# Performance work log

Measured on AMD Instinct MI355X. Metric: run time of the kernel, lower is better.

The kernel has to match this reference:

```python
import jax, jax.numpy as jnp
import numpy as np

N_VIEW = 4
N_USER = 1_000_000
N_PRODUCT = 500_000
EMB = 64


def setup_inputs() -> dict:
    key = jax.random.key(0)
    k1, k2, k3, k4 = jax.random.split(key, 4)
    return {
        "view_users": jax.random.normal(k1, (N_VIEW, N_USER, EMB), dtype=jnp.float32),
        "view_products": jax.random.normal(k2, (N_VIEW, N_PRODUCT, EMB), dtype=jnp.float32),
        "user_view_weight": jax.random.normal(k3, (1, N_VIEW), dtype=jnp.float32),
        "product_view_weight": jax.random.normal(k4, (1, N_VIEW), dtype=jnp.float32),
    }


def reference(view_users, view_products, user_view_weight, product_view_weight):
    # softmax over the view axis (dim=1 of the [1, n_view] weight)
    uw = jax.nn.softmax(user_view_weight, axis=1)[0]      # [n_view]
    pw = jax.nn.softmax(product_view_weight, axis=1)[0]   # [n_view]
    # fused weighted sum over views: sum_v w[v] * items[v]
    users = jnp.einsum("v,vne->ne", uw, view_users)       # [n_user, emb]
    products = jnp.einsum("v,vme->me", pw, view_products) # [n_product, emb]
    return (users, products)
```

## Files before the change

### kernel.cpp

```cpp
#include <hip/hip_runtime.h>


typedef float f4 __attribute__((ext_vector_type(4)));

constexpr long long N_USER = 1000000LL;
constexpr long long N_PRODUCT = 500000LL;
constexpr int EMB = 64;

constexpr int BLOCK = 256;
constexpr int GRID = 2048;
constexpr int STRIDE = BLOCK * GRID;
constexpr int NU4 = (int)(N_USER * EMB / 4);
constexpr int NP4 = (int)(N_PRODUCT * EMB / 4);
constexpr int U_ITERS = NU4 / STRIDE;
constexpr int U_REM = NU4 % STRIDE;
constexpr int P_ITERS = NP4 / STRIDE;
constexpr int P_REM = NP4 % STRIDE;

__global__ __launch_bounds__(BLOCK) void fused_view_sum(
    const float* __restrict__ vu,
    const float* __restrict__ vp,
    const float* __restrict__ uwp,
    const float* __restrict__ pwp,
    float* __restrict__ out)
{
    float u0 = uwp[0], u1 = uwp[1], u2 = uwp[2], u3 = uwp[3];
    float um = fmaxf(fmaxf(u0, u1), fmaxf(u2, u3));
    float ue0 = expf(u0 - um), ue1 = expf(u1 - um), ue2 = expf(u2 - um), ue3 = expf(u3 - um);
    float uinv = 1.0f / (ue0 + ue1 + ue2 + ue3);
    const float w0 = ue0 * uinv, w1 = ue1 * uinv, w2 = ue2 * uinv, w3 = ue3 * uinv;

    float p0 = pwp[0], p1 = pwp[1], p2 = pwp[2], p3 = pwp[3];
    float pm = fmaxf(fmaxf(p0, p1), fmaxf(p2, p3));
    float pe0 = expf(p0 - pm), pe1 = expf(p1 - pm), pe2 = expf(p2 - pm), pe3 = expf(p3 - pm);
    float pinv = 1.0f / (pe0 + pe1 + pe2 + pe3);
    const float q0 = pe0 * pinv, q1 = pe1 * pinv, q2 = pe2 * pinv, q3 = pe3 * pinv;

    const int tid = blockIdx.x * BLOCK + threadIdx.x;

    const f4* __restrict__ vu4 = (const f4*)vu;
    const f4* __restrict__ vp4 = (const f4*)vp;
    f4* __restrict__ ou4 = (f4*)out;
    f4* __restrict__ op4 = (f4*)(out + N_USER * EMB);

#pragma unroll 2
    for (int k = 0; k < U_ITERS; ++k) {
        const int i = tid + k * STRIDE;
        f4 a = __builtin_nontemporal_load(vu4 + i);
        f4 b = __builtin_nontemporal_load(vu4 + i + NU4);
        f4 c = __builtin_nontemporal_load(vu4 + i + 2 * NU4);
        f4 d = __builtin_nontemporal_load(vu4 + i + 3 * NU4);
        f4 r = w0 * a + w1 * b + w2 * c + w3 * d;
        __builtin_nontemporal_store(r, ou4 + i);
    }
    if (tid < U_REM) {
        const int i = tid + U_ITERS * STRIDE;
        f4 a = __builtin_nontemporal_load(vu4 + i);
        f4 b = __builtin_nontemporal_load(vu4 + i + NU4);
        f4 c = __builtin_nontemporal_load(vu4 + i + 2 * NU4);
        f4 d = __builtin_nontemporal_load(vu4 + i + 3 * NU4);
        f4 r = w0 * a + w1 * b + w2 * c + w3 * d;
        __builtin_nontemporal_store(r, ou4 + i);
    }

#pragma unroll 2
    for (int k = 0; k < P_ITERS; ++k) {
        const int j = tid + k * STRIDE;
        f4 a = __builtin_nontemporal_load(vp4 + j);
        f4 b = __builtin_nontemporal_load(vp4 + j + NP4);
        f4 c = __builtin_nontemporal_load(vp4 + j + 2 * NP4);
        f4 d = __builtin_nontemporal_load(vp4 + j + 3 * NP4);
        f4 r = q0 * a + q1 * b + q2 * c + q3 * d;
        __builtin_nontemporal_store(r, op4 + j);
    }
    if (tid < P_REM) {
        const int j = tid + P_ITERS * STRIDE;
        f4 a = __builtin_nontemporal_load(vp4 + j);
        f4 b = __builtin_nontemporal_load(vp4 + j + NP4);
        f4 c = __builtin_nontemporal_load(vp4 + j + 2 * NP4);
        f4 d = __builtin_nontemporal_load(vp4 + j + 3 * NP4);
        f4 r = q0 * a + q1 * b + q2 * c + q3 * d;
        __builtin_nontemporal_store(r, op4 + j);
    }
}

extern "C" void kernel_launch(void* const* d_in, const int* in_sizes, int n_in,
                              void* d_out, int out_size, void* d_ws, size_t ws_size,
                              hipStream_t stream) {
    const float* vu = (const float*)d_in[0];
    const float* vp = (const float*)d_in[1];
    const float* uw = (const float*)d_in[2];
    const float* pw = (const float*)d_in[3];
    float* out = (float*)d_out;

    fused_view_sum<<<GRID, BLOCK, 0, stream>>>(vu, vp, uw, pw, out);
}
```

Measured before the change: 390.0 us.

## Process wave-sized chunks per view batch with unified user/product loop

Each wave now owns contiguous groups of 512 float4 elements and issues eight loads per view before accumulating. User and product work is merged into one flat wave-level loop. This aims to increase memory-level parallelism and balance work across waves, at the cost of higher register use. Output stores also switch from nontemporal to ordinary stores, which changes cache behaviour.

Result: faster. 368.5 us (-5.5%).

```diff
diff --git a/kernel.cpp b/kernel.cpp
--- a/kernel.cpp
+++ b/kernel.cpp
@@ -9,13 +9,14 @@
 
 constexpr int BLOCK = 256;
 constexpr int GRID = 2048;
-constexpr int STRIDE = BLOCK * GRID;
+constexpr int NWAVES = GRID * (BLOCK / 64);
+constexpr int JPT = 8;
+constexpr int GSIZE = 64 * JPT;
 constexpr int NU4 = (int)(N_USER * EMB / 4);
 constexpr int NP4 = (int)(N_PRODUCT * EMB / 4);
-constexpr int U_ITERS = NU4 / STRIDE;
-constexpr int U_REM = NU4 % STRIDE;
-constexpr int P_ITERS = NP4 / STRIDE;
-constexpr int P_REM = NP4 % STRIDE;
+constexpr int UG = NU4 / GSIZE;
+constexpr int PG = NP4 / GSIZE;
+constexpr int TG = UG + PG;
 
 __global__ __launch_bounds__(BLOCK) void fused_view_sum(
     const float* __restrict__ vu,
@@ -36,51 +37,47 @@
     float pinv = 1.0f / (pe0 + pe1 + pe2 + pe3);
     const float q0 = pe0 * pinv, q1 = pe1 * pinv, q2 = pe2 * pinv, q3 = pe3 * pinv;
 
-    const int tid = blockIdx.x * BLOCK + threadIdx.x;
+    const int flat = blockIdx.x * BLOCK + threadIdx.x;
+    const int wave = flat >> 6;
+    const int lane = flat & 63;
 
     const f4* __restrict__ vu4 = (const f4*)vu;
     const f4* __restrict__ vp4 = (const f4*)vp;
     f4* __restrict__ ou4 = (f4*)out;
     f4* __restrict__ op4 = (f4*)(out + N_USER * EMB);
 
-#pragma unroll 2
-    for (int k = 0; k < U_ITERS; ++k) {
-        const int i = tid + k * STRIDE;
-        f4 a = __builtin_nontemporal_load(vu4 + i);
-        f4 b = __builtin_nontemporal_load(vu4 + i + NU4);
-        f4 c = __builtin_nontemporal_load(vu4 + i + 2 * NU4);
-        f4 d = __builtin_nontemporal_load(vu4 + i + 3 * NU4);
-        f4 r = w0 * a + w1 * b + w2 * c + w3 * d;
-        __builtin_nontemporal_store(r, ou4 + i);
-    }
-    if (tid < U_REM) {
-        const int i = tid + U_ITERS * STRIDE;
-        f4 a = __builtin_nontemporal_load(vu4 + i);
-        f4 b = __builtin_nontemporal_load(vu4 + i + NU4);
-        f4 c = __builtin_nontemporal_load(vu4 + i + 2 * NU4);
-        f4 d = __builtin_nontemporal_load(vu4 + i + 3 * NU4);
-        f4 r = w0 * a + w1 * b + w2 * c + w3 * d;
-        __builtin_nontemporal_store(r, ou4 + i);
-    }
+    for (int g = wave; g < TG; g += NWAVES) {
+        const bool isU = g < UG;
+        const f4* __restrict__ src = isU ? vu4 : vp4;
+        f4* __restrict__ dst = isU ? ou4 : op4;
+        const int stride = isU ? NU4 : NP4;
+        const int base = (isU ? g : g - UG) * GSIZE + lane;
+        const float c0 = isU ? w0 : q0;
+        const float c1 = isU ? w1 : q1;
+        const float c2 = isU ? w2 : q2;
+        const float c3 = isU ? w3 : q3;
 
-#pragma unroll 2
-    for (int k = 0; k < P_ITERS; ++k) {
-        const int j = tid + k * STRIDE;
-        f4 a = __builtin_nontemporal_load(vp4 + j);
-        f4 b = __builtin_nontemporal_load(vp4 + j + NP4);
-        f4 c = __builtin_nontemporal_load(vp4 + j + 2 * NP4);
-        f4 d = __builtin_nontemporal_load(vp4 + j + 3 * NP4);
-        f4 r = q0 * a + q1 * b + q2 * c + q3 * d;
-        __builtin_nontemporal_store(r, op4 + j);
-    }
-    if (tid < P_REM) {
-        const int j = tid + P_ITERS * STRIDE;
-        f4 a = __builtin_nontemporal_load(vp4 + j);
-        f4 b = __builtin_nontemporal_load(vp4 + j + NP4);
-        f4 c = __builtin_nontemporal_load(vp4 + j + 2 * NP4);
-        f4 d = __builtin_nontemporal_load(vp4 + j + 3 * NP4);
-        f4 r = q0 * a + q1 * b + q2 * c + q3 * d;
-        __builtin_nontemporal_store(r, op4 + j);
+        f4 acc[JPT];
+        f4 t[JPT];
+
+#pragma unroll
+        for (int j = 0; j < JPT; ++j) t[j] = __builtin_nontemporal_load(src + base + j * 64);
+#pragma unroll
+        for (int j = 0; j < JPT; ++j) acc[j] = c0 * t[j];
+#pragma unroll
+        for (int j = 0; j < JPT; ++j) t[j] = __builtin_nontemporal_load(src + stride + base + j * 64);
+#pragma unroll
+        for (int j = 0; j < JPT; ++j) acc[j] += c1 * t[j];
+#pragma unroll
+        for (int j = 0; j < JPT; ++j) t[j] = __builtin_nontemporal_load(src + 2 * stride + base + j * 64);
+#pragma unroll
+        for (int j = 0; j < JPT; ++j) acc[j] += c2 * t[j];
+#pragma unroll
+        for (int j = 0; j < JPT; ++j) t[j] = __builtin_nontemporal_load(src + 3 * stride + base + j * 64);
+#pragma unroll
+        for (int j = 0; j < JPT; ++j) acc[j] += c3 * t[j];
+#pragma unroll
+        for (int j = 0; j < JPT; ++j) dst[base + j * 64] = acc[j];
     }
 }
 
```
